# Kernel tuning notes

Measured on AMD Instinct MI355X. Metric: run time of the kernel, lower is better.

Reference implementation:

```python
import jax, jax.numpy as jnp
from jax import lax
import numpy as np

WIN_SIZE = 11
WIN_SIGMA = 1.5
DATA_RANGE = 1.0
K1, K2 = 0.01, 0.03
DN = ('NCHW', 'OIHW', 'NCHW')


def _gauss_1d(size, sigma):
    coords = jnp.arange(size, dtype=jnp.float32) - (size // 2)
    g = jnp.exp(-coords ** 2 / (2.0 * sigma ** 2))
    return g / g.sum()


def _gaussian_filter(x, g):
    # depthwise separable valid conv: along W then along H (order irrelevant)
    C = x.shape[1]
    kw = jnp.tile(g.reshape(1, 1, 1, -1), (C, 1, 1, 1))  # [C,1,1,K]
    kh = jnp.tile(g.reshape(1, 1, -1, 1), (C, 1, 1, 1))  # [C,1,K,1]
    x = lax.conv_general_dilated(x, kw, (1, 1), 'VALID',
                                 feature_group_count=C, dimension_numbers=DN)
    x = lax.conv_general_dilated(x, kh, (1, 1), 'VALID',
                                 feature_group_count=C, dimension_numbers=DN)
    return x


def setup_inputs() -> dict:
    key = jax.random.key(0)
    k1, k2 = jax.random.split(key)
    X = jax.random.uniform(k1, (32, 3, 512, 512), dtype=jnp.float32, minval=-1.0, maxval=1.0)
    Y = jax.random.uniform(k2, (32, 3, 512, 512), dtype=jnp.float32, minval=-1.0, maxval=1.0)
    return {"X": X, "Y": Y}


def reference(X, Y):
    # channel == 3 -> normalize from [-1,1] to [0,1]
    X = (X + 1.0) / 2.0
    Y = (Y + 1.0) / 2.0

    g = _gauss_1d(WIN_SIZE, WIN_SIGMA).astype(X.dtype)
    C1 = (K1 * DATA_RANGE) ** 2
    C2 = (K2 * DATA_RANGE) ** 2

    mu1 = _gaussian_filter(X, g)
    mu2 = _gaussian_filter(Y, g)
    mu1_sq = mu1 * mu1
    mu2_sq = mu2 * mu2
    mu1_mu2 = mu1 * mu2

    sigma1_sq = _gaussian_filter(X * X, g) - mu1_sq
    sigma2_sq = _gaussian_filter(Y * Y, g) - mu2_sq
    sigma12 = _gaussian_filter(X * Y, g) - mu1_mu2

    cs_map = (2.0 * sigma12 + C2) / (sigma1_sq + sigma2_sq + C2)
    ssim_map = (2.0 * mu1_mu2 + C1) / (mu1_sq + mu2_sq + C1) * cs_map

    # size_average=True, full=False -> scalar mean SSIM
    return ssim_map.mean()
```

## Files before the change

### kernel.cpp

```cpp
#include <hip/hip_runtime.h>
#include <cmath>


#define HH 512
#define WW 512
#define OH 502
#define OW 502
#define NC 96
#define TXS 32
#define TYB 64
#define INR 74
#define HP4 33
#define GX 16
#define GY 8
#define NTASK (INR * 8)
#define NSLOT 64

typedef float f4 __attribute__((ext_vector_type(4)));

struct GaussW { float g[11]; };

static __device__ __forceinline__ f4 sp(float s) { return (f4){s, s, s, s}; }

__global__ __launch_bounds__(256, 4) void ssim_kernel(
        const float* __restrict__ X, const float* __restrict__ Y,
        double* __restrict__ acc, GaussW gw) {
    __shared__ f4 hS[INR][HP4];
    __shared__ double wsum[4];

    const int tid = threadIdx.x;
    const int R0 = blockIdx.y * TYB;
    const int C0 = blockIdx.x * TXS;
    const float* Xp = X + (size_t)blockIdx.z * (HH * WW);
    const float* Yp = Y + (size_t)blockIdx.z * (HH * WW);
    const bool edge = (blockIdx.x == GX - 1);

    for (int t = tid; t < NTASK; t += 256) {
        int r, cg;
        if (t < 576) { r = (t & 7) | ((t >> 6) << 3); cg = (t >> 3) & 7; }
        else         { int tt = t - 576; r = 72 + (tt & 1); cg = (tt >> 1) & 7; }
        const int gr = min(R0 + r, HH - 1);
        const float* xrow = Xp + gr * WW;
        const float* yrow = Yp + gr * WW;
        const int gc = C0 + 4 * cg;

        float xv[16], yv[16];
        if (!edge) {
            const float4* x4 = (const float4*)(xrow + gc);
            const float4* y4 = (const float4*)(yrow + gc);
            float4 a0 = x4[0], a1 = x4[1], a2 = x4[2], a3 = x4[3];
            float4 b0 = y4[0], b1 = y4[1], b2 = y4[2], b3 = y4[3];
            xv[0]=a0.x; xv[1]=a0.y; xv[2]=a0.z; xv[3]=a0.w;
            xv[4]=a1.x; xv[5]=a1.y; xv[6]=a1.z; xv[7]=a1.w;
            xv[8]=a2.x; xv[9]=a2.y; xv[10]=a2.z; xv[11]=a2.w;
            xv[12]=a3.x; xv[13]=a3.y; xv[14]=a3.z; xv[15]=a3.w;
            yv[0]=b0.x; yv[1]=b0.y; yv[2]=b0.z; yv[3]=b0.w;
            yv[4]=b1.x; yv[5]=b1.y; yv[6]=b1.z; yv[7]=b1.w;
            yv[8]=b2.x; yv[9]=b2.y; yv[10]=b2.z; yv[11]=b2.w;
            yv[12]=b3.x; yv[13]=b3.y; yv[14]=b3.z; yv[15]=b3.w;
        } else {
            #pragma unroll
            for (int i = 0; i < 16; ++i) {
                int c = min(gc + i, WW - 1);
                xv[i] = xrow[c];
                yv[i] = yrow[c];
            }
        }

        f4 a0v = sp(0.f), a1v = sp(0.f), a2v = sp(0.f), a3v = sp(0.f);
        #pragma unroll
        for (int k = 0; k < 14; ++k) {
            float x = xv[k], y = yv[k];
            f4 P;
            P.x = x; P.y = y;
            P.z = fmaf(x, x, y * y);
            P.w = x * y;
            #pragma unroll
            for (int j = 0; j < 4; ++j) {
                int u = k - j;
                if (u >= 0 && u < 11) {
                    f4 G = sp(gw.g[u]);
                    if (j == 0) a0v = __builtin_elementwise_fma(G, P, a0v);
                    if (j == 1) a1v = __builtin_elementwise_fma(G, P, a1v);
                    if (j == 2) a2v = __builtin_elementwise_fma(G, P, a2v);
                    if (j == 3) a3v = __builtin_elementwise_fma(G, P, a3v);
                }
            }
        }
        hS[r][4 * cg + 0] = a0v;
        hS[r][4 * cg + 1] = a1v;
        hS[r][4 * cg + 2] = a2v;
        hS[r][4 * cg + 3] = a3v;
    }
    __syncthreads();

    const int c  = tid & 31;
    const int rb = (tid >> 5) * 8;
    f4 A[8];
    #pragma unroll
    for (int j = 0; j < 8; ++j) A[j] = sp(0.f);
    #pragma unroll
    for (int k = 0; k < 18; ++k) {
        f4 v = hS[rb + k][c];
        #pragma unroll
        for (int j = 0; j < 8; ++j) {
            int u = k - j;
            if (u >= 0 && u < 11) {
                f4 G = sp(gw.g[u]);
                A[j] = __builtin_elementwise_fma(G, v, A[j]);
            }
        }
    }

    const float C1 = 1.0e-4f;
    const float C2 = 9.0e-4f;
    float nn[8], dd[8];
    #pragma unroll
    for (int j = 0; j < 8; ++j) {
        f4 v = A[j];
        float t1 = v.x + 1.f, t2 = v.y + 1.f;
        float num1 = fmaf(t1 * t2, 0.5f, C1);
        float den1 = fmaf(fmaf(t2, t2, t1 * t1), 0.25f, C1);
        float num2 = fmaf(v.w - v.x * v.y, 0.5f, C2);
        float den2 = fmaf(v.z - fmaf(v.x, v.x, v.y * v.y), 0.25f, C2);
        bool valid = (R0 + rb + j < OH) & (C0 + c < OW);
        nn[j] = valid ? num1 * num2 : 0.f;
        dd[j] = valid ? den1 * den2 : 1.f;
    }
    double tsum = 0.0;
    #pragma unroll
    for (int g = 0; g < 8; g += 4) {
        float d01 = dd[g] * dd[g + 1], d23 = dd[g + 2] * dd[g + 3];
        float s01 = fmaf(nn[g], dd[g + 1], nn[g + 1] * dd[g]);
        float s23 = fmaf(nn[g + 2], dd[g + 3], nn[g + 3] * dd[g + 2]);
        tsum += (double)(fmaf(s01, d23, s23 * d01) / (d01 * d23));
    }

    #pragma unroll
    for (int off = 32; off > 0; off >>= 1)
        tsum += __shfl_down(tsum, off, 64);
    if ((tid & 63) == 0) wsum[tid >> 6] = tsum;
    __syncthreads();
    if (tid == 0) {
        int slot = (blockIdx.x + blockIdx.y * GX + blockIdx.z * GX * GY) & (NSLOT - 1);
        atomicAdd(&acc[slot * 8], wsum[0] + wsum[1] + wsum[2] + wsum[3]);
    }
}

__global__ void ssim_finalize(const double* __restrict__ acc,
                              float* __restrict__ out) {
    int lane = threadIdx.x;
    double t = acc[lane * 8];
    #pragma unroll
    for (int off = 32; off > 0; off >>= 1)
        t += __shfl_down(t, off, 64);
    if (lane == 0)
        out[0] = (float)(t * (1.0 / (double)((long long)NC * OH * OW)));
}

extern "C" void kernel_launch(void* const* d_in, const int* in_sizes, int n_in,
                              void* d_out, int out_size, void* d_ws, size_t ws_size,
                              hipStream_t stream) {
    const float* X = (const float*)d_in[0];
    const float* Y = (const float*)d_in[1];
    float* out = (float*)d_out;
    double* acc = (double*)d_ws;

    hipMemsetAsync(d_ws, 0, NSLOT * 64, stream);

    GaussW gw;
    {
        double g[11], s = 0.0;
        for (int i = 0; i < 11; ++i) {
            double d = (double)(i - 5);
            g[i] = exp(-d * d / (2.0 * 1.5 * 1.5));
            s += g[i];
        }
        for (int i = 0; i < 11; ++i) gw.g[i] = (float)(g[i] / s);
    }

    dim3 grid(GX, GY, NC);
    ssim_kernel<<<grid, dim3(256), 0, stream>>>(X, Y, acc, gw);
    ssim_finalize<<<1, dim3(64), 0, stream>>>(acc, out);
}
```

Measured before the change: 293.7 us.

## Shrink row tile to 54 so each thread does exactly two horizontal tasks

Changes the block row tile from 64 to 54 output rows (64 input rows), so the horizontal pass is exactly 512 tasks and each thread handles two, with all four row loads issued up front before the convolutions. The vertical pass now computes 7 rows per thread over 17 taps instead of 8 over 18. The in-wave reduction switches from double to float shuffles. In exchange the grid grows to 10 row blocks, a larger fraction of loaded rows is halo overhead, and the last row group has idle work.

```diff
diff --git a/kernel.cpp b/kernel.cpp
--- a/kernel.cpp
+++ b/kernel.cpp
@@ -8,12 +8,11 @@
 #define OW 502
 #define NC 96
 #define TXS 32
-#define TYB 64
-#define INR 74
+#define TYB 54
+#define INR 64
 #define HP4 33
 #define GX 16
-#define GY 8
-#define NTASK (INR * 8)
+#define GY 10
 #define NSLOT 64
 
 typedef float f4 __attribute__((ext_vector_type(4)));
@@ -22,11 +21,54 @@
 
 static __device__ __forceinline__ f4 sp(float s) { return (f4){s, s, s, s}; }
 
+static __device__ __forceinline__ void load16(float* v, const float* p) {
+    const float4* q = (const float4*)p;
+    float4 a = q[0], b = q[1], c = q[2], d = q[3];
+    v[0]=a.x;  v[1]=a.y;  v[2]=a.z;  v[3]=a.w;
+    v[4]=b.x;  v[5]=b.y;  v[6]=b.z;  v[7]=b.w;
+    v[8]=c.x;  v[9]=c.y;  v[10]=c.z; v[11]=c.w;
+    v[12]=d.x; v[13]=d.y; v[14]=d.z; v[15]=d.w;
+}
+
+static __device__ __forceinline__ void load16c(float* v, const float* row, int gc) {
+    #pragma unroll
+    for (int i = 0; i < 16; ++i)
+        v[i] = row[min(gc + i, WW - 1)];
+}
+
+static __device__ __forceinline__ void conv_store(f4 (*hS)[HP4], const GaussW& gw,
+        int r, int cg, const float* xv, const float* yv) {
+    f4 a0 = sp(0.f), a1 = sp(0.f), a2 = sp(0.f), a3 = sp(0.f);
+    #pragma unroll
+    for (int k = 0; k < 14; ++k) {
+        float x = xv[k], y = yv[k];
+        f4 P;
+        P.x = x; P.y = y;
+        P.z = fmaf(x, x, y * y);
+        P.w = x * y;
+        #pragma unroll
+        for (int j = 0; j < 4; ++j) {
+            int u = k - j;
+            if (u >= 0 && u < 11) {
+                f4 G = sp(gw.g[u]);
+                if (j == 0) a0 = __builtin_elementwise_fma(G, P, a0);
+                if (j == 1) a1 = __builtin_elementwise_fma(G, P, a1);
+                if (j == 2) a2 = __builtin_elementwise_fma(G, P, a2);
+                if (j == 3) a3 = __builtin_elementwise_fma(G, P, a3);
+            }
+        }
+    }
+    hS[r][4 * cg + 0] = a0;
+    hS[r][4 * cg + 1] = a1;
+    hS[r][4 * cg + 2] = a2;
+    hS[r][4 * cg + 3] = a3;
+}
+
 __global__ __launch_bounds__(256, 4) void ssim_kernel(
         const float* __restrict__ X, const float* __restrict__ Y,
         double* __restrict__ acc, GaussW gw) {
     __shared__ f4 hS[INR][HP4];
-    __shared__ double wsum[4];
+    __shared__ float wsum[4];
 
     const int tid = threadIdx.x;
     const int R0 = blockIdx.y * TYB;
@@ -35,75 +77,39 @@
     const float* Yp = Y + (size_t)blockIdx.z * (HH * WW);
     const bool edge = (blockIdx.x == GX - 1);
 
-    for (int t = tid; t < NTASK; t += 256) {
-        int r, cg;
-        if (t < 576) { r = (t & 7) | ((t >> 6) << 3); cg = (t >> 3) & 7; }
-        else         { int tt = t - 576; r = 72 + (tt & 1); cg = (tt >> 1) & 7; }
-        const int gr = min(R0 + r, HH - 1);
-        const float* xrow = Xp + gr * WW;
-        const float* yrow = Yp + gr * WW;
-        const int gc = C0 + 4 * cg;
+    const int t0 = tid, t1 = tid + 256;
+    const int r0 = (t0 & 7) | ((t0 >> 6) << 3), cg0 = (t0 >> 3) & 7;
+    const int r1 = (t1 & 7) | ((t1 >> 6) << 3), cg1 = (t1 >> 3) & 7;
+    const int gr0 = min(R0 + r0, HH - 1);
+    const int gr1 = min(R0 + r1, HH - 1);
+    const int gc0 = C0 + 4 * cg0, gc1 = C0 + 4 * cg1;
 
-        float xv[16], yv[16];
-        if (!edge) {
-            const float4* x4 = (const float4*)(xrow + gc);
-            const float4* y4 = (const float4*)(yrow + gc);
-            float4 a0 = x4[0], a1 = x4[1], a2 = x4[2], a3 = x4[3];
-            float4 b0 = y4[0], b1 = y4[1], b2 = y4[2], b3 = y4[3];
-            xv[0]=a0.x; xv[1]=a0.y; xv[2]=a0.z; xv[3]=a0.w;
-            xv[4]=a1.x; xv[5]=a1.y; xv[6]=a1.z; xv[7]=a1.w;
-            xv[8]=a2.x; xv[9]=a2.y; xv[10]=a2.z; xv[11]=a2.w;
-            xv[12]=a3.x; xv[13]=a3.y; xv[14]=a3.z; xv[15]=a3.w;
-            yv[0]=b0.x; yv[1]=b0.y; yv[2]=b0.z; yv[3]=b0.w;
-            yv[4]=b1.x; yv[5]=b1.y; yv[6]=b1.z; yv[7]=b1.w;
-            yv[8]=b2.x; yv[9]=b2.y; yv[10]=b2.z; yv[11]=b2.w;
-            yv[12]=b3.x; yv[13]=b3.y; yv[14]=b3.z; yv[15]=b3.w;
-        } else {
-            #pragma unroll
-            for (int i = 0; i < 16; ++i) {
-                int c = min(gc + i, WW - 1);
-                xv[i] = xrow[c];
-                yv[i] = yrow[c];
-            }
-        }
-
-        f4 a0v = sp(0.f), a1v = sp(0.f), a2v = sp(0.f), a3v = sp(0.f);
-        #pragma unroll
-        for (int k = 0; k < 14; ++k) {
-            float x = xv[k], y = yv[k];
-            f4 P;
-            P.x = x; P.y = y;
-            P.z = fmaf(x, x, y * y);
-            P.w = x * y;
-            #pragma unroll
-            for (int j = 0; j < 4; ++j) {
-                int u = k - j;
-                if (u >= 0 && u < 11) {
-                    f4 G = sp(gw.g[u]);
-                    if (j == 0) a0v = __builtin_elementwise_fma(G, P, a0v);
-                    if (j == 1) a1v = __builtin_elementwise_fma(G, P, a1v);
-                    if (j == 2) a2v = __builtin_elementwise_fma(G, P, a2v);
-                    if (j == 3) a3v = __builtin_elementwise_fma(G, P, a3v);
-                }
-            }
-        }
-        hS[r][4 * cg + 0] = a0v;
-        hS[r][4 * cg + 1] = a1v;
-        hS[r][4 * cg + 2] = a2v;
-        hS[r][4 * cg + 3] = a3v;
+    float xv0[16], yv0[16], xv1[16], yv1[16];
+    if (!edge) {
+        load16(xv0, Xp + gr0 * WW + gc0);
+        load16(yv0, Yp + gr0 * WW + gc0);
+        load16(xv1, Xp + gr1 * WW + gc1);
+        load16(yv1, Yp + gr1 * WW + gc1);
+    } else {
+        load16c(xv0, Xp + gr0 * WW, gc0);
+        load16c(yv0, Yp + gr0 * WW, gc0);
+        load16c(xv1, Xp + gr1 * WW, gc1);
+        load16c(yv1, Yp + gr1 * WW, gc1);
     }
+    conv_store(hS, gw, r0, cg0, xv0, yv0);
+    conv_store(hS, gw, r1, cg1, xv1, yv1);
     __syncthreads();
 
     const int c  = tid & 31;
-    const int rb = (tid >> 5) * 8;
-    f4 A[8];
+    const int rb = (tid >> 5) * 7;
+    f4 A[7];
     #pragma unroll
-    for (int j = 0; j < 8; ++j) A[j] = sp(0.f);
+    for (int j = 0; j < 7; ++j) A[j] = sp(0.f);
     #pragma unroll
-    for (int k = 0; k < 18; ++k) {
-        f4 v = hS[rb + k][c];
+    for (int k = 0; k < 17; ++k) {
+        f4 v = hS[min(rb + k, INR - 1)][c];
         #pragma unroll
-        for (int j = 0; j < 8; ++j) {
+        for (int j = 0; j < 7; ++j) {
             int u = k - j;
             if (u >= 0 && u < 11) {
                 f4 G = sp(gw.g[u]);
@@ -114,27 +120,28 @@
 
     const float C1 = 1.0e-4f;
     const float C2 = 9.0e-4f;
-    float nn[8], dd[8];
+    float nn[7], dd[7];
     #pragma unroll
-    for (int j = 0; j < 8; ++j) {
+    for (int j = 0; j < 7; ++j) {
         f4 v = A[j];
-        float t1 = v.x + 1.f, t2 = v.y + 1.f;
-        float num1 = fmaf(t1 * t2, 0.5f, C1);
-        float den1 = fmaf(fmaf(t2, t2, t1 * t1), 0.25f, C1);
+        float t1f = v.x + 1.f, t2f = v.y + 1.f;
+        float num1 = fmaf(t1f * t2f, 0.5f, C1);
+        float den1 = fmaf(fmaf(t2f, t2f, t1f * t1f), 0.25f, C1);
         float num2 = fmaf(v.w - v.x * v.y, 0.5f, C2);
         float den2 = fmaf(v.z - fmaf(v.x, v.x, v.y * v.y), 0.25f, C2);
-        bool valid = (R0 + rb + j < OH) & (C0 + c < OW);
+        int row = rb + j;
+        bool valid = (row < TYB) & (R0 + row < OH) & (C0 + c < OW);
         nn[j] = valid ? num1 * num2 : 0.f;
         dd[j] = valid ? den1 * den2 : 1.f;
     }
-    double tsum = 0.0;
-    #pragma unroll
-    for (int g = 0; g < 8; g += 4) {
-        float d01 = dd[g] * dd[g + 1], d23 = dd[g + 2] * dd[g + 3];
-        float s01 = fmaf(nn[g], dd[g + 1], nn[g + 1] * dd[g]);
-        float s23 = fmaf(nn[g + 2], dd[g + 3], nn[g + 3] * dd[g + 2]);
-        tsum += (double)(fmaf(s01, d23, s23 * d01) / (d01 * d23));
-    }
+    float d01 = dd[0] * dd[1], d23 = dd[2] * dd[3];
+    float s01 = fmaf(nn[0], dd[1], nn[1] * dd[0]);
+    float s23 = fmaf(nn[2], dd[3], nn[3] * dd[2]);
+    float tA  = fmaf(s01, d23, s23 * d01) / (d01 * d23);
+    float d45 = dd[4] * dd[5];
+    float s45 = fmaf(nn[4], dd[5], nn[5] * dd[4]);
+    float tB  = fmaf(s45, dd[6], nn[6] * d45) / (d45 * dd[6]);
+    float tsum = tA + tB;
 
     #pragma unroll
     for (int off = 32; off > 0; off >>= 1)
@@ -142,8 +149,10 @@
     if ((tid & 63) == 0) wsum[tid >> 6] = tsum;
     __syncthreads();
     if (tid == 0) {
+        double t = (double)wsum[0] + (double)wsum[1]
+                 + (double)wsum[2] + (double)wsum[3];
         int slot = (blockIdx.x + blockIdx.y * GX + blockIdx.z * GX * GY) & (NSLOT - 1);
-        atomicAdd(&acc[slot * 8], wsum[0] + wsum[1] + wsum[2] + wsum[3]);
+        atomicAdd(&acc[slot * 8], t);
     }
 }
 
```

After: 305.5 us. 1.04x slower.
